# Kernel optimization log

Measured on AMD Instinct MI355X. Metric: run time of the kernel, lower is better.

The kernel has to match this reference:

```python
import jax, jax.numpy as jnp
import numpy as np

H = 12  # num_heads

def _alibi_bias(num_heads, n, dtype):
    # slopes: ratio**i for i in 1..H, ratio = 2**(-8/H)
    ratio = 2.0 ** (-8.0 / num_heads)
    slopes = ratio ** jnp.arange(1, num_heads + 1, dtype=jnp.float32)  # [H]
    pos = jnp.arange(n)
    rel = jnp.abs(pos[None, :] - pos[:, None]).astype(jnp.float32)  # [N,N]
    return (-slopes[:, None, None] * rel[None]).astype(dtype)  # [H,N,N]

def setup_inputs() -> dict:
    key = jax.random.key(0)
    ks = jax.random.split(key, 5)
    B, N, C = 16, 1024, 768
    s = 0.02
    return {
        "x": jax.random.normal(ks[0], (B, N, C), jnp.float32),
        "w_qkv": jax.random.normal(ks[1], (3 * C, C), jnp.float32) * s,
        "b_qkv": jax.random.normal(ks[2], (3 * C,), jnp.float32) * s,
        "w_proj": jax.random.normal(ks[3], (C, C), jnp.float32) * s,
        "b_proj": jax.random.normal(ks[4], (C,), jnp.float32) * s,
    }

def reference(x, w_qkv, b_qkv, w_proj, b_proj):
    B, N, C = x.shape
    D = C // H
    scale = D ** -0.5
    qkv = x @ w_qkv.T + b_qkv                       # [B,N,3C]
    qkv = qkv.reshape(B, N, 3, H, D)
    q = qkv[:, :, 0].transpose(0, 2, 1, 3)          # [B,H,N,D]
    k = qkv[:, :, 1].transpose(0, 2, 1, 3)
    v = qkv[:, :, 2].transpose(0, 2, 1, 3)
    bias = _alibi_bias(H, N, x.dtype)               # [H,N,N]
    scores = jnp.einsum('bhnd,bhmd->bhnm', q, k) * scale + bias[None]
    attn = jax.nn.softmax(scores, axis=-1)
    out = jnp.einsum('bhnm,bhmd->bhnd', attn, v)    # [B,H,N,D]
    out = out.transpose(0, 2, 1, 3).reshape(B, N, C)
    return out @ w_proj.T + b_proj
```

## Files before the change

kernel.cpp:

```cpp
#include <hip/hip_runtime.h>


typedef unsigned short u16;
typedef unsigned int u32;
typedef __attribute__((ext_vector_type(8))) short short8;
typedef __attribute__((ext_vector_type(4))) float f32x4;

__device__ __forceinline__ u16 f2bf(float f) {
    u32 u = __float_as_uint(f);
    u32 r = u + 0x7FFFu + ((u >> 16) & 1u);
    return (u16)(r >> 16);
}

__device__ __forceinline__ f32x4 mfma16(short8 a, short8 b, f32x4 c) {
    return __builtin_amdgcn_mfma_f32_16x16x32_bf16(a, b, c, 0, 0, 0);
}
__device__ __forceinline__ u32 cvtpk_bf16(float lo, float hi) {
    u32 r;
    asm("v_cvt_pk_bf16_f32 %0, %1, %2" : "=v"(r) : "v"(lo), "v"(hi));
    return r;
}

typedef __attribute__((address_space(1))) const unsigned int gu32_t;
typedef __attribute__((address_space(3))) unsigned int su32_t;
__device__ __forceinline__ void gl16(const u16* g, u16* s) {
    __builtin_amdgcn_global_load_lds((gu32_t*)g, (su32_t*)s, 16, 0, 0);
}

__global__ void cvt_all(const float* __restrict__ x, const float* __restrict__ wq,
                        const float* __restrict__ wp, u16* __restrict__ Xb,
                        u16* __restrict__ Wqkvb, u16* __restrict__ Wprojb) {
    int i = blockIdx.x * blockDim.x + threadIdx.x;
    int stride = gridDim.x * blockDim.x;
    for (int idx = i; idx < 3735552; idx += stride) {
        const float* src;
        u16* dst;
        int k;
        if (idx < 3145728) { src = x; dst = Xb; k = idx; }
        else if (idx < 3588096) { src = wq; dst = Wqkvb; k = idx - 3145728; }
        else { src = wp; dst = Wprojb; k = idx - 3588096; }
        float4 v = *(const float4*)(src + (size_t)k * 4);
        ushort4 o;
        o.x = f2bf(v.x); o.y = f2bf(v.y); o.z = f2bf(v.z); o.w = f2bf(v.w);
        *(ushort4*)(dst + (size_t)k * 4) = o;
    }
}

template <int EPI>
__global__ __launch_bounds__(512) void gemm_nt(
    const u16* __restrict__ A, const u16* __restrict__ Bw,
    const float* __restrict__ bias, u16* __restrict__ outb, float* __restrict__ outf,
    int nTilesN)
{
    constexpr int K = 768;
    constexpr int nkt = K / 32;
    __shared__ __align__(16) u16 lA[3][128 * 32];
    __shared__ __align__(16) u16 lB[3][128 * 32];

    int tid = threadIdx.x;
    int bid = blockIdx.x;
    int nwg = gridDim.x;
    int cpx = nwg >> 3;
    int swz = (bid & 7) * cpx + (bid >> 3);
    int bm = swz / nTilesN;
    int bn = swz - bm * nTilesN;
    int m0 = bm * 128, n0 = bn * 128;

    int sr = tid >> 2;
    int sc = (tid & 3) << 3;
    const u16* pA = A + (size_t)(m0 + sr) * K + sc;
    const u16* pB = Bw + (size_t)(n0 + sr) * K + sc;
    int lo = tid * 8;

    gl16(pA,      &lA[0][lo]);
    gl16(pB,      &lB[0][lo]);
    gl16(pA + 32, &lA[1][lo]);
    gl16(pB + 32, &lB[1][lo]);

    int w = tid >> 6, lane = tid & 63;
    int wm = w >> 2, wn = w & 3;
    int fq = lane >> 4, fr = lane & 15;
    f32x4 acc[4][2] = {};

    for (int kt = 0; kt < nkt; ++kt) {
        int cur = kt % 3;
        if (kt < nkt - 1) { asm volatile("s_waitcnt vmcnt(2)" ::: "memory"); }
        else              { asm volatile("s_waitcnt vmcnt(0)" ::: "memory"); }
        __builtin_amdgcn_sched_barrier(0);
        __builtin_amdgcn_s_barrier();
        __builtin_amdgcn_sched_barrier(0);
        if (kt + 2 < nkt) {
            int nx = (kt + 2) % 3;
            gl16(pA + (kt + 2) * 32, &lA[nx][lo]);
            gl16(pB + (kt + 2) * 32, &lB[nx][lo]);
        }
        short8 af[4], bfr[2];
#pragma unroll
        for (int i = 0; i < 4; ++i)
            af[i] = *(const short8*)&lA[cur][(wm * 64 + i * 16 + fr) * 32 + fq * 8];
#pragma unroll
        for (int j = 0; j < 2; ++j)
            bfr[j] = *(const short8*)&lB[cur][(wn * 32 + j * 16 + fr) * 32 + fq * 8];
        __builtin_amdgcn_s_setprio(1);
#pragma unroll
        for (int i = 0; i < 4; ++i)
#pragma unroll
            for (int j = 0; j < 2; ++j)
                acc[i][j] = mfma16(af[i], bfr[j], acc[i][j]);
        __builtin_amdgcn_s_setprio(0);
    }

    if (EPI == 0) {
        int b = m0 >> 10;
        int i0 = (m0 & 1023) + wm * 64;
#pragma unroll
        for (int j = 0; j < 2; ++j) {
            int colb = n0 + wn * 32 + j * 16;
            int s = colb / 768;
            int rem = colb % 768;
            int hh = rem >> 6;
            int d0 = rem & 63;
            float bval = bias[colb + fr];
            u16* obase = outb + (((size_t)s * 16 + b) * 12 + hh) * 65536;
#pragma unroll
            for (int i = 0; i < 4; ++i) {
                int r0 = i0 + i * 16 + fq * 4;
#pragma unroll
                for (int r = 0; r < 4; ++r)
                    obase[(size_t)(r0 + r) * 64 + d0 + fr] = f2bf(acc[i][j][r] + bval);
            }
        }
    } else {
#pragma unroll
        for (int j = 0; j < 2; ++j) {
            int col = n0 + wn * 32 + j * 16 + fr;
            float bval = bias[col];
#pragma unroll
            for (int i = 0; i < 4; ++i) {
                int row0 = m0 + wm * 64 + i * 16 + fq * 4;
#pragma unroll
                for (int r = 0; r < 4; ++r)
                    outf[(size_t)(row0 + r) * 768 + col] = acc[i][j][r] + bval;
            }
        }
    }
}

__global__ __launch_bounds__(256) void attn_alibi(
    const u16* __restrict__ QKV, u16* __restrict__ att)
{
    int g = blockIdx.x;
    int xcd = g & 7;
    int idx = g >> 3;
    int qt = idx & 15;
    int bh = xcd * 24 + (idx >> 4);
    int h = bh % 12;
    int b = bh / 12;
    int q0 = qt * 64;
    const u16* Qg = QKV + (size_t)bh * 65536;
    const u16* Kg = QKV + (size_t)(192 + bh) * 65536;
    const u16* Vg = QKV + (size_t)(384 + bh) * 65536;

    __shared__ __align__(16) u16 Ks[64][72];
    __shared__ __align__(16) u16 Vt[64][72];
    __shared__ __align__(16) u16 Ps[64][72];

    int tid = threadIdx.x, w = tid >> 6, lane = tid & 63;
    int fq = lane >> 4, fr = lane & 15;

    short8 aq0 = *(const short8*)(Qg + (size_t)(q0 + w * 16 + fr) * 64 + fq * 8);
    short8 aq1 = *(const short8*)(Qg + (size_t)(q0 + w * 16 + fr) * 64 + 32 + fq * 8);

    const float C1 = 0.125f * 1.44269504f;
    float c2 = __builtin_amdgcn_exp2f(-(2.0f / 3.0f) * (float)(h + 1)) * 1.44269504f;
    int distThr = (int)(40.0f / c2);
    int lo_kv = q0 - 63 - distThr;
    int hi_kv = q0 + 63 + distThr;
    int t_lo = (lo_kv <= 0) ? 0 : (lo_kv >> 6);
    int t_hi = (hi_kv >= 1023) ? 15 : (hi_kv >> 6);

    int sr0 = tid >> 3;
    int sr1 = sr0 + 32;
    int vk0 = sr0 * 2;
    int sc = (tid & 7) * 8;
    int vswz = (tid & 7) << 3;

    uint4 kr0 = *(const uint4*)(Kg + (size_t)(t_lo * 64 + sr0) * 64 + sc);
    uint4 kr1 = *(const uint4*)(Kg + (size_t)(t_lo * 64 + sr1) * 64 + sc);
    uint4 vr0 = *(const uint4*)(Vg + (size_t)(t_lo * 64 + vk0) * 64 + sc);
    uint4 vr1 = *(const uint4*)(Vg + (size_t)(t_lo * 64 + vk0 + 1) * 64 + sc);

    float di = (float)(q0 + w * 16 + fr - fq * 4);
    float lsum = 0.f;
    f32x4 acc[4] = {};

    for (int it = t_lo; it <= t_hi; ++it) {
        __syncthreads();
        *(uint4*)&Ks[sr0][sc] = kr0;
        *(uint4*)&Ks[sr1][sc] = kr1;
        {
            const u16* v0 = (const u16*)&vr0;
            const u16* v1 = (const u16*)&vr1;
            int col = vk0 ^ vswz;
#pragma unroll
            for (int jj = 0; jj < 8; ++jj)
                *(u32*)&Vt[sc + jj][col] = (u32)v0[jj] | ((u32)v1[jj] << 16);
        }
        __syncthreads();

        if (it < t_hi) {
            int kvn = (it + 1) * 64;
            kr0 = *(const uint4*)(Kg + (size_t)(kvn + sr0) * 64 + sc);
            kr1 = *(const uint4*)(Kg + (size_t)(kvn + sr1) * 64 + sc);
            vr0 = *(const uint4*)(Vg + (size_t)(kvn + vk0) * 64 + sc);
            vr1 = *(const uint4*)(Vg + (size_t)(kvn + vk0 + 1) * 64 + sc);
        }

        f32x4 sfr[4];
        __builtin_amdgcn_s_setprio(1);
#pragma unroll
        for (int ct = 0; ct < 4; ++ct) {
            short8 bk0 = *(const short8*)&Ks[ct * 16 + fr][fq * 8];
            short8 bk1 = *(const short8*)&Ks[ct * 16 + fr][32 + fq * 8];
            f32x4 s0 = {0.f, 0.f, 0.f, 0.f};
            s0 = mfma16(bk0, aq0, s0);
            s0 = mfma16(bk1, aq1, s0);
            sfr[ct] = s0;
        }
        __builtin_amdgcn_s_setprio(0);

        float dkv = di - (float)(it * 64);
#pragma unroll
        for (int ct = 0; ct < 4; ++ct) {
            float t0 = dkv - (float)(ct * 16);
            float e0 = __builtin_amdgcn_exp2f(fmaf(sfr[ct][0], C1, -c2 * fabsf(t0)));
            float e1 = __builtin_amdgcn_exp2f(fmaf(sfr[ct][1], C1, -c2 * fabsf(t0 - 1.0f)));
            float e2 = __builtin_amdgcn_exp2f(fmaf(sfr[ct][2], C1, -c2 * fabsf(t0 - 2.0f)));
            float e3 = __builtin_amdgcn_exp2f(fmaf(sfr[ct][3], C1, -c2 * fabsf(t0 - 3.0f)));
            lsum += (e0 + e1) + (e2 + e3);
            uint2 pk;
            pk.x = cvtpk_bf16(e0, e1);
            pk.y = cvtpk_bf16(e2, e3);
            *(uint2*)&Ps[w * 16 + fr][ct * 16 + fq * 4] = pk;
        }

        short8 pa0 = *(const short8*)&Ps[w * 16 + fr][fq * 8];
        short8 pa1 = *(const short8*)&Ps[w * 16 + fr][32 + fq * 8];
        __builtin_amdgcn_s_setprio(1);
#pragma unroll
        for (int dt = 0; dt < 4; ++dt) {
            int row = dt * 16 + fr;
            int swzr = (row >> 3) << 3;
            short8 bv0 = *(const short8*)&Vt[row][(fq * 8) ^ swzr];
            short8 bv1 = *(const short8*)&Vt[row][(32 + fq * 8) ^ swzr];
            acc[dt] = mfma16(pa0, bv0, acc[dt]);
            acc[dt] = mfma16(pa1, bv1, acc[dt]);
        }
        __builtin_amdgcn_s_setprio(0);
    }

    float l = lsum;
    l += __shfl_xor(l, 16);
    l += __shfl_xor(l, 32);
    float rlo = 1.0f / l;
    float rl[4];
#pragma unroll
    for (int r = 0; r < 4; ++r)
        rl[r] = __shfl(rlo, fq * 4 + r);

#pragma unroll
    for (int dt = 0; dt < 4; ++dt)
#pragma unroll
        for (int r = 0; r < 4; ++r) {
            int ig = q0 + w * 16 + fq * 4 + r;
            att[((size_t)(b * 1024 + ig) * 12 + h) * 64 + dt * 16 + fr] =
                (u16)cvtpk_bf16(acc[dt][r] * rl[r], 0.f);
        }
}

extern "C" void kernel_launch(void* const* d_in, const int* in_sizes, int n_in,
                              void* d_out, int out_size, void* d_ws, size_t ws_size,
                              hipStream_t stream) {
    const float* x      = (const float*)d_in[0];
    const float* w_qkv  = (const float*)d_in[1];
    const float* b_qkv  = (const float*)d_in[2];
    const float* w_proj = (const float*)d_in[3];
    const float* b_proj = (const float*)d_in[4];
    float* out = (float*)d_out;

    char* ws = (char*)d_ws;
    u16* Xb     = (u16*)ws;
    u16* Wqkvb  = (u16*)(ws + 25165824);
    u16* Wprojb = (u16*)(ws + 28704768);
    u16* QKVb   = (u16*)(ws + 29884416);
    u16* Attb   = Xb;

    cvt_all<<<2048, 256, 0, stream>>>(x, w_qkv, w_proj, Xb, Wqkvb, Wprojb);

    gemm_nt<0><<<128 * 18, 512, 0, stream>>>(Xb, Wqkvb, b_qkv, QKVb, nullptr, 18);
    attn_alibi<<<3072, 256, 0, stream>>>(QKVb, Attb);
    gemm_nt<1><<<128 * 6, 512, 0, stream>>>(Attb, Wprojb, b_proj, nullptr, out, 6);
}
```

Measured before the change: 193.3 us.

## Process 128 query rows per attention block with split K/V loaders

Doubles the query tile per attention block to 128 rows using 512 threads, so each staged K/V tile is shared by twice as many queries and global K/V traffic drops. Half the threads load K and the other half load and transpose V, instead of every thread doing both. The KV window grows slightly to cover the wider query range, and the larger block with more LDS use may reduce occupancy and raise wasted tile work near the window edges.

```diff
diff --git a/kernel.cpp b/kernel.cpp
--- a/kernel.cpp
+++ b/kernel.cpp
@@ -146,24 +146,24 @@
     }
 }
 
-__global__ __launch_bounds__(256) void attn_alibi(
+__global__ __launch_bounds__(512) void attn_alibi(
     const u16* __restrict__ QKV, u16* __restrict__ att)
 {
     int g = blockIdx.x;
     int xcd = g & 7;
     int idx = g >> 3;
-    int qt = idx & 15;
-    int bh = xcd * 24 + (idx >> 4);
+    int qt = idx & 7;
+    int bh = xcd * 24 + (idx >> 3);
     int h = bh % 12;
     int b = bh / 12;
-    int q0 = qt * 64;
+    int q0 = qt * 128;
     const u16* Qg = QKV + (size_t)bh * 65536;
     const u16* Kg = QKV + (size_t)(192 + bh) * 65536;
     const u16* Vg = QKV + (size_t)(384 + bh) * 65536;
 
     __shared__ __align__(16) u16 Ks[64][72];
     __shared__ __align__(16) u16 Vt[64][72];
-    __shared__ __align__(16) u16 Ps[64][72];
+    __shared__ __align__(16) u16 Ps[128][72];
 
     int tid = threadIdx.x, w = tid >> 6, lane = tid & 63;
     int fq = lane >> 4, fr = lane & 15;
@@ -175,20 +175,24 @@
     float c2 = __builtin_amdgcn_exp2f(-(2.0f / 3.0f) * (float)(h + 1)) * 1.44269504f;
     int distThr = (int)(40.0f / c2);
     int lo_kv = q0 - 63 - distThr;
-    int hi_kv = q0 + 63 + distThr;
+    int hi_kv = q0 + 127 + distThr;
     int t_lo = (lo_kv <= 0) ? 0 : (lo_kv >> 6);
     int t_hi = (hi_kv >= 1023) ? 15 : (hi_kv >> 6);
 
-    int sr0 = tid >> 3;
-    int sr1 = sr0 + 32;
+    bool isK = tid < 256;
+    int t2 = tid & 255;
+    int sr0 = t2 >> 3;
+    int sc = (t2 & 7) * 8;
+    int vswz = (t2 & 7) << 3;
     int vk0 = sr0 * 2;
-    int sc = (tid & 7) * 8;
-    int vswz = (tid & 7) << 3;
-
-    uint4 kr0 = *(const uint4*)(Kg + (size_t)(t_lo * 64 + sr0) * 64 + sc);
-    uint4 kr1 = *(const uint4*)(Kg + (size_t)(t_lo * 64 + sr1) * 64 + sc);
-    uint4 vr0 = *(const uint4*)(Vg + (size_t)(t_lo * 64 + vk0) * 64 + sc);
-    uint4 vr1 = *(const uint4*)(Vg + (size_t)(t_lo * 64 + vk0 + 1) * 64 + sc);
+    int vcol = vk0 ^ vswz;
+    const u16* g0 = isK ? (Kg + (size_t)sr0 * 64 + sc)
+                        : (Vg + (size_t)vk0 * 64 + sc);
+    const u16* g1 = isK ? (Kg + (size_t)(sr0 + 32) * 64 + sc)
+                        : (Vg + (size_t)(vk0 + 1) * 64 + sc);
+
+    uint4 r0 = *(const uint4*)(g0 + (size_t)t_lo * 4096);
+    uint4 r1 = *(const uint4*)(g1 + (size_t)t_lo * 4096);
 
     float di = (float)(q0 + w * 16 + fr - fq * 4);
     float lsum = 0.f;
@@ -196,24 +200,21 @@
 
     for (int it = t_lo; it <= t_hi; ++it) {
         __syncthreads();
-        *(uint4*)&Ks[sr0][sc] = kr0;
-        *(uint4*)&Ks[sr1][sc] = kr1;
-        {
-            const u16* v0 = (const u16*)&vr0;
-            const u16* v1 = (const u16*)&vr1;
-            int col = vk0 ^ vswz;
+        if (isK) {
+            *(uint4*)&Ks[sr0][sc] = r0;
+            *(uint4*)&Ks[sr0 + 32][sc] = r1;
+        } else {
+            const u16* v0 = (const u16*)&r0;
+            const u16* v1 = (const u16*)&r1;
 #pragma unroll
             for (int jj = 0; jj < 8; ++jj)
-                *(u32*)&Vt[sc + jj][col] = (u32)v0[jj] | ((u32)v1[jj] << 16);
+                *(u32*)&Vt[sc + jj][vcol] = (u32)v0[jj] | ((u32)v1[jj] << 16);
         }
         __syncthreads();
 
         if (it < t_hi) {
-            int kvn = (it + 1) * 64;
-            kr0 = *(const uint4*)(Kg + (size_t)(kvn + sr0) * 64 + sc);
-            kr1 = *(const uint4*)(Kg + (size_t)(kvn + sr1) * 64 + sc);
-            vr0 = *(const uint4*)(Vg + (size_t)(kvn + vk0) * 64 + sc);
-            vr1 = *(const uint4*)(Vg + (size_t)(kvn + vk0 + 1) * 64 + sc);
+            r0 = *(const uint4*)(g0 + (size_t)(it + 1) * 4096);
+            r1 = *(const uint4*)(g1 + (size_t)(it + 1) * 4096);
         }
 
         f32x4 sfr[4];
@@ -298,6 +299,6 @@
     cvt_all<<<2048, 256, 0, stream>>>(x, w_qkv, w_proj, Xb, Wqkvb, Wprojb);
 
     gemm_nt<0><<<128 * 18, 512, 0, stream>>>(Xb, Wqkvb, b_qkv, QKVb, nullptr, 18);
-    attn_alibi<<<3072, 256, 0, stream>>>(QKVb, Attb);
+    attn_alibi<<<1536, 512, 0, stream>>>(QKVb, Attb);
     gemm_nt<1><<<128 * 6, 512, 0, stream>>>(Attb, Wprojb, b_proj, nullptr, out, 6);
 }
```

Measured after the change: 190.3 us (median of 2 runs). Within noise of the previous version (-1.6%).
